# Kernel tuning notes

Measured on AMD Instinct MI355X. Metric: run time of the kernel, lower is better.

## Reference

```python
import jax, jax.numpy as jnp
import numpy as np

B, S, D, H = 2, 2048, 1024, 16
DH = D // H

def setup_inputs() -> dict:
    key = jax.random.key(0)
    ks = jax.random.split(key, 9)
    s = 1.0 / np.sqrt(D)
    def lin(k):
        kw, kb = jax.random.split(k)
        W = jax.random.uniform(kw, (D, D), jnp.float32, -s, s)
        b = jax.random.uniform(kb, (D,), jnp.float32, -s, s)
        return W, b
    Wq, bq = lin(ks[0]); Wk, bk = lin(ks[1]); Wv, bv = lin(ks[2]); Wo, bo = lin(ks[3])
    x = jax.random.normal(ks[4], (B, S, D), jnp.float32)
    return {"x": x, "Wq": Wq, "bq": bq, "Wk": Wk, "bk": bk,
            "Wv": Wv, "bv": bv, "Wo": Wo, "bo": bo}

def _split_heads(t):
    # [B,S,D] -> [B,H,S,DH]
    return t.reshape(B, S, H, DH).transpose(0, 2, 1, 3)

def reference(x, Wq, bq, Wk, bk, Wv, bv, Wo, bo):
    # torch Linear: y = x @ W.T + b
    q = _split_heads(x @ Wq.T + bq)
    k = _split_heads(x @ Wk.T + bk)
    v = _split_heads(x @ Wv.T + bv)
    scores = jnp.einsum('bhqd,bhkd->bhqk', q, k) / jnp.sqrt(jnp.float32(DH))
    p = jax.nn.softmax(scores, axis=-1)  # dropout is identity in eval
    o = jnp.einsum('bhqk,bhkd->bhqd', p, v)
    o = o.transpose(0, 2, 1, 3).reshape(B, S, D)  # combine heads
    return o @ Wo.T + bo
```

## Files before the change

### kernel.cpp

```cpp
#include <hip/hip_runtime.h>


typedef __bf16 bf16;
typedef bf16 bf16x8 __attribute__((ext_vector_type(8)));
typedef bf16 bf16x4 __attribute__((ext_vector_type(4)));
typedef short s16x4 __attribute__((ext_vector_type(4)));
typedef float f32x4 __attribute__((ext_vector_type(4)));

#define MFMA32(a, b, c) __builtin_amdgcn_mfma_f32_16x16x32_bf16(a, b, c, 0, 0, 0)

#if __has_builtin(__builtin_amdgcn_mfma_f32_16x16x16bf16_1k)
#define HAVE_MFMA16 1
#define MFMA16(a, b, c) __builtin_amdgcn_mfma_f32_16x16x16bf16_1k(a, b, c, 0, 0, 0)
#else
#define HAVE_MFMA16 0
#endif

#define GLL(g, l) __builtin_amdgcn_global_load_lds(                              \
    (const __attribute__((address_space(1))) void*)(const void*)(g),             \
    (__attribute__((address_space(3))) void*)(void*)(l), 16, 0, 0)

union pk4 { bf16x4 h; s16x4 s; unsigned int d[2]; };
union v8u { bf16x8 v; bf16x4 h[2]; s16x4 s[2]; };

__global__ __launch_bounds__(256)
void cvt_bf16(const float* __restrict__ x,  const float* __restrict__ Wq,
              const float* __restrict__ Wk, const float* __restrict__ Wv,
              const float* __restrict__ Wo,
              bf16* __restrict__ xb, bf16* __restrict__ wqb, bf16* __restrict__ wkb,
              bf16* __restrict__ wvb, bf16* __restrict__ wob)
{
    const int idx = blockIdx.x * 256 + threadIdx.x;
    const float* src; bf16* dst; int off;
    if (idx < 1048576) { src = x; dst = xb; off = idx; }
    else {
        const int r = idx - 1048576;
        const int seg = r >> 18;
        off = r & 262143;
        src = (seg == 0) ? Wq : (seg == 1) ? Wk : (seg == 2) ? Wv : Wo;
        dst = (seg == 0) ? wqb : (seg == 1) ? wkb : (seg == 2) ? wvb : wob;
    }
    const float4 v = ((const float4*)src)[off];
    bf16x4 o = {(bf16)v.x, (bf16)v.y, (bf16)v.z, (bf16)v.w};
    *(bf16x4*)(dst + (size_t)off * 4) = o;
}

__global__ __launch_bounds__(256, 3)
void qkv_gemm(const bf16* __restrict__ xb,
              const bf16* __restrict__ wqb, const float* __restrict__ bq,
              const bf16* __restrict__ wkb, const float* __restrict__ bk,
              const bf16* __restrict__ wvb, const float* __restrict__ bv,
              bf16* __restrict__ q_ws, bf16* __restrict__ k_ws, bf16* __restrict__ v_ws)
{
    const int z = blockIdx.z;
    const bf16*  W    = (z == 0) ? wqb : (z == 1) ? wkb : wvb;
    const float* bias = (z == 0) ? bq  : (z == 1) ? bk  : bv;

    __shared__ bf16 As[128][64];
    __shared__ bf16 Bs[128][64];
    __shared__ char ebuf[17408];
    bf16 (*Et)[68]  = (bf16(*)[68])ebuf;
    bf16 (*Vt)[132] = (bf16(*)[132])ebuf;

    const int m0 = blockIdx.x * 128;
    const int n0 = blockIdx.y * 128;
    const int t    = threadIdx.x;
    const int wave = t >> 6;
    const int lane = t & 63;
    const int lr   = lane & 15;
    const int quad = lane >> 4;
    const int wm = (wave & 1) * 64;
    const int wn = (wave >> 1) * 64;

    const int srow8 = lane >> 3;
    const int pcol  = (lane & 7) * 8;
    const int gcol  = ((lane & 7) ^ (lane >> 3)) * 8;
    const bf16* gaU[4]; const bf16* gbU[4]; bf16* laU[4]; bf16* lbU[4];
    #pragma unroll
    for (int u = 0; u < 4; u++) {
        const int row = wave * 32 + u * 8 + srow8;
        gaU[u] = xb + (size_t)(m0 + row) * 1024 + gcol;
        gbU[u] = W  + (size_t)(n0 + row) * 1024 + gcol;
        laU[u] = &As[row][pcol];
        lbU[u] = &Bs[row][pcol];
    }
    const int swA = (lr & 7) * 8;

    f32x4 acc[4][4] = {};

    for (int k0 = 0; k0 < 1024; k0 += 64) {
        #pragma unroll
        for (int u = 0; u < 4; u++) {
            GLL(gaU[u] + k0, laU[u]);
            GLL(gbU[u] + k0, lbU[u]);
        }
        __syncthreads();

        bf16x8 af[4][2], bfr[4][2];
        #pragma unroll
        for (int i = 0; i < 4; i++)
            #pragma unroll
            for (int kc = 0; kc < 2; kc++)
                af[i][kc] = *(const bf16x8*)&As[wm + i*16 + lr][(kc*32 + quad*8) ^ swA];
        #pragma unroll
        for (int j = 0; j < 4; j++)
            #pragma unroll
            for (int kc = 0; kc < 2; kc++)
                bfr[j][kc] = *(const bf16x8*)&Bs[wn + j*16 + lr][(kc*32 + quad*8) ^ swA];
        #pragma unroll
        for (int kc = 0; kc < 2; kc++)
            #pragma unroll
            for (int i = 0; i < 4; i++)
                #pragma unroll
                for (int j = 0; j < 4; j++)
                    acc[i][j] = MFMA32(af[i][kc], bfr[j][kc], acc[i][j]);
        __syncthreads();
    }

    const int bi = m0 >> 11, si0 = m0 & 2047;
    if (z < 2) {
        bf16* hw = (z == 0) ? q_ws : k_ws;
        const float sc = (z == 0) ? 0.125f : 1.0f;
        #pragma unroll
        for (int ph = 0; ph < 2; ph++) {
            if ((wave >> 1) == ph) {
                #pragma unroll
                for (int j = 0; j < 4; j++) {
                    const float bb = bias[n0 + ph * 64 + j * 16 + lr];
                    #pragma unroll
                    for (int i = 0; i < 4; i++)
                        #pragma unroll
                        for (int r = 0; r < 4; r++)
                            Et[wm + i*16 + quad*4 + r][j*16 + lr] =
                                (bf16)((acc[i][j][r] + bb) * sc);
                }
            }
            __syncthreads();
            const int hh = (n0 >> 6) + ph;
            bf16* dst = hw + (((size_t)bi * 16 + hh) * 2048 + si0) * 64;
            const int row = t >> 1, cc = (t & 1) * 32;
            #pragma unroll
            for (int e = 0; e < 4; e++)
                *(bf16x8*)(dst + (size_t)row * 64 + cc + e * 8) =
                    *(const bf16x8*)&Et[row][cc + e * 8];
            __syncthreads();
        }
    } else {
        #pragma unroll
        for (int ph = 0; ph < 2; ph++) {
            if ((wave >> 1) == ph) {
                #pragma unroll
                for (int j = 0; j < 4; j++) {
                    const float bb = bias[n0 + ph * 64 + j * 16 + lr];
                    #pragma unroll
                    for (int i = 0; i < 4; i++)
                        #pragma unroll
                        for (int r = 0; r < 4; r++)
                            Vt[j * 16 + lr][wm + i * 16 + quad * 4 + r] =
                                (bf16)(acc[i][j][r] + bb);
                }
            }
            __syncthreads();
            const int c  = t >> 2;
            const int sc_ = (t & 3) * 32;
            const int col = n0 + ph * 64 + c;
            const int h = col >> 6, dh = col & 63;
            bf16* dst = v_ws + (((size_t)bi * 16 + h) * 64 + dh) * 2048 + si0 + sc_;
            #pragma unroll
            for (int e = 0; e < 4; e++)
                *(bf16x8*)(dst + e * 8) = *(const bf16x8*)&Vt[c][sc_ + e * 8];
            __syncthreads();
        }
    }
}

__global__ __launch_bounds__(256, 4)
void attn(const bf16* __restrict__ q_ws, const bf16* __restrict__ k_ws,
          const bf16* __restrict__ v_ws, bf16* __restrict__ o_ws)
{
    const int qt = blockIdx.x;
    const int bh = blockIdx.y;
    const int b_ = bh >> 4, h = bh & 15;

    const bf16* qbase = q_ws + (size_t)bh * 2048 * 64;
    const bf16* kbase = k_ws + (size_t)bh * 2048 * 64;
    const bf16* vbase = v_ws + (size_t)bh * 64 * 2048;

    __shared__ bf16 Ks[128][72];
    __shared__ bf16 Vs[64][136];

    const int t    = threadIdx.x;
    const int wave = t >> 6;
    const int lane = t & 63;
    const int lr   = lane & 15;
    const int quad = lane >> 4;

    bf16x8 aq[2];
    #pragma unroll
    for (int kc = 0; kc < 2; kc++)
        aq[kc] = *(const bf16x8*)(qbase +
            (size_t)(qt*64 + wave*16 + lr) * 64 + kc*32 + quad*8);

    float m_i = -1e30f, l_i = 0.f;
    f32x4 o_accT[4] = {};
    const float C = 1.44269504f;
    const s16x4 ones = {0x3F80, 0x3F80, 0x3F80, 0x3F80};

    bf16x8 kreg[4], vreg[4];
    #pragma unroll
    for (int u = 0; u < 4; u++) {
        const int c = t + u * 256;
        kreg[u] = *(const bf16x8*)(kbase + (size_t)c * 8);
        vreg[u] = *(const bf16x8*)(vbase + (size_t)(c >> 4) * 2048 + (c & 15) * 8);
    }

    for (int kt = 0; kt < 16; kt++) {
        __syncthreads();
        #pragma unroll
        for (int u = 0; u < 4; u++) {
            const int c = t + u * 256;
            *(bf16x8*)&Ks[c >> 3][(c & 7) * 8] = kreg[u];
#if HAVE_MFMA16
            const int d = c >> 4, k_ = c & 15;
            const int lo = (k_ & 1) * 64 + (k_ >> 1) * 4;
            v8u vv; vv.v = vreg[u];
            *(bf16x4*)&Vs[d][lo]      = vv.h[0];
            *(bf16x4*)&Vs[d][lo + 32] = vv.h[1];
#else
            *(bf16x8*)&Vs[c >> 4][(c & 15) * 8] = vreg[u];
#endif
        }
        __syncthreads();
        if (kt < 15) {
            #pragma unroll
            for (int u = 0; u < 4; u++) {
                const int c = t + u * 256;
                kreg[u] = *(const bf16x8*)(kbase + (size_t)(kt+1) * 8192 + c * 8);
                vreg[u] = *(const bf16x8*)(vbase + (size_t)(c >> 4) * 2048
                                           + (kt+1) * 128 + (c & 15) * 8);
            }
        }

        f32x4 sacc[8];
        #pragma unroll
        for (int j = 0; j < 8; j++) {
            bf16x8 kf0 = *(const bf16x8*)&Ks[j*16 + lr][quad*8];
            bf16x8 kf1 = *(const bf16x8*)&Ks[j*16 + lr][32 + quad*8];
            f32x4 a = {0.f, 0.f, 0.f, 0.f};
            a = MFMA32(kf0, aq[0], a);
            a = MFMA32(kf1, aq[1], a);
            sacc[j] = a;
        }

        float m = -1e30f;
        #pragma unroll
        for (int j = 0; j < 8; j++)
            #pragma unroll
            for (int r = 0; r < 4; r++) m = fmaxf(m, sacc[j][r]);
        m = fmaxf(m, __shfl_xor(m, 16));
        m = fmaxf(m, __shfl_xor(m, 32));
        const float nm = fmaxf(m_i, m);
        const float al = exp2f((m_i - nm) * C);
        m_i = nm;
        const float nmc = nm * C;
        #pragma unroll
        for (int n = 0; n < 4; n++)
            #pragma unroll
            for (int r = 0; r < 4; r++) o_accT[n][r] *= al;

#if HAVE_MFMA16
        f32x4 lacc = {0.f, 0.f, 0.f, 0.f};
        #pragma unroll
        for (int c4 = 0; c4 < 4; c4++) {
            v8u vf[4];
            #pragma unroll
            for (int fb = 0; fb < 4; fb++)
                vf[fb].v = *(const bf16x8*)&Vs[fb*16 + lr][quad*32 + c4*8];
            #pragma unroll
            for (int jj = 0; jj < 2; jj++) {
                const int j = c4*2 + jj;
                pk4 pf;
                pf.h = bf16x4{
                    (bf16)exp2f(fmaf(sacc[j][0], C, -nmc)),
                    (bf16)exp2f(fmaf(sacc[j][1], C, -nmc)),
                    (bf16)exp2f(fmaf(sacc[j][2], C, -nmc)),
                    (bf16)exp2f(fmaf(sacc[j][3], C, -nmc))};
                #pragma unroll
                for (int fb = 0; fb < 4; fb++)
                    o_accT[fb] = MFMA16(vf[fb].s[jj], pf.s, o_accT[fb]);
                lacc = MFMA16(ones, pf.s, lacc);
            }
        }
        l_i = l_i * al + lacc[0];
#else
        float rs = 0.f;
        #pragma unroll
        for (int j = 0; j < 8; j++)
            #pragma unroll
            for (int r = 0; r < 4; r++) {
                const float p = exp2f(fmaf(sacc[j][r], C, -nmc));
                sacc[j][r] = p;
                rs += p;
            }
        rs += __shfl_xor(rs, 16);
        rs += __shfl_xor(rs, 32);
        l_i = l_i * al + rs;
        unsigned int p0[8], p1[8];
        #pragma unroll
        for (int j = 0; j < 8; j++) {
            pk4 pf;
            pf.h = bf16x4{(bf16)sacc[j][0], (bf16)sacc[j][1],
                          (bf16)sacc[j][2], (bf16)sacc[j][3]};
            p0[j] = pf.d[0]; p1[j] = pf.d[1];
        }
        const int srcA = lr + 16 * ((2 * quad) & 3);
        const int srcB = lr + 16 * ((2 * quad + 1) & 3);
        const bool hi = (quad >> 1) != 0;
        #pragma unroll
        for (int c = 0; c < 4; c++) {
            unsigned int a0 = __shfl(p0[2*c], srcA), a1 = __shfl(p0[2*c+1], srcA);
            unsigned int b0 = __shfl(p1[2*c], srcA), b1 = __shfl(p1[2*c+1], srcA);
            unsigned int c0 = __shfl(p0[2*c], srcB), c1 = __shfl(p0[2*c+1], srcB);
            unsigned int d0 = __shfl(p1[2*c], srcB), d1 = __shfl(p1[2*c+1], srcB);
            unsigned int fr[4];
            fr[0] = hi ? a1 : a0;
            fr[1] = hi ? b1 : b0;
            fr[2] = hi ? c1 : c0;
            fr[3] = hi ? d1 : d0;
            bf16x8 pf8 = *(bf16x8*)fr;
            #pragma unroll
            for (int fb = 0; fb < 4; fb++) {
                bf16x8 vf8 = *(const bf16x8*)&Vs[fb*16 + lr][c*32 + quad*8];
                o_accT[fb] = MFMA32(vf8, pf8, o_accT[fb]);
            }
        }
#endif
    }

    __syncthreads();
    bf16 (*OsE)[68] = (bf16(*)[68])&Ks[0][0];
    const float inv = 1.0f / l_i;
    const int sil = wave * 16 + lr;
    #pragma unroll
    for (int fb = 0; fb < 4; fb++)
        #pragma unroll
        for (int r = 0; r < 4; r++)
            OsE[sil][fb*16 + quad*4 + r] = (bf16)(o_accT[fb][r] * inv);
    __syncthreads();
    const int row = t >> 2, seg = (t & 3) * 16;
    bf16* dst = o_ws + ((size_t)b_ * 2048 + qt*64 + row) * 1024 + h*64 + seg;
    *(bf16x8*)(dst)     = *(const bf16x8*)&OsE[row][seg];
    *(bf16x8*)(dst + 8) = *(const bf16x8*)&OsE[row][seg + 8];
}

__global__ __launch_bounds__(256, 3)
void out_gemm(const bf16* __restrict__ o_ws,
              const bf16* __restrict__ wob, const float* __restrict__ bo,
              float* __restrict__ out)
{
    __shared__ bf16 As[64][64];
    __shared__ bf16 Bs[128][64];
    __shared__ float Ot[64][68];

    const int m0 = blockIdx.x * 64;
    const int n0 = blockIdx.y * 128;
    const int t    = threadIdx.x;
    const int wave = t >> 6;
    const int lane = t & 63;
    const int lr   = lane & 15;
    const int quad = lane >> 4;
    const int wm = (wave & 1) * 32;
    const int wn = (wave >> 1) * 64;

    const int srow8 = lane >> 3;
    const int pcol  = (lane & 7) * 8;
    const int gcol  = ((lane & 7) ^ (lane >> 3)) * 8;
    const bf16* gaU[2]; bf16* laU[2];
    #pragma unroll
    for (int u = 0; u < 2; u++) {
        const int row = wave * 16 + u * 8 + srow8;
        gaU[u] = o_ws + (size_t)(m0 + row) * 1024 + gcol;
        laU[u] = &As[row][pcol];
    }
    const bf16* gbU[4]; bf16* lbU[4];
    #pragma unroll
    for (int u = 0; u < 4; u++) {
        const int row = wave * 32 + u * 8 + srow8;
        gbU[u] = wob + (size_t)(n0 + row) * 1024 + gcol;
        lbU[u] = &Bs[row][pcol];
    }
    const int swA = (lr & 7) * 8;

    f32x4 acc[2][4] = {};

    for (int k0 = 0; k0 < 1024; k0 += 64) {
        #pragma unroll
        for (int u = 0; u < 2; u++) GLL(gaU[u] + k0, laU[u]);
        #pragma unroll
        for (int u = 0; u < 4; u++) GLL(gbU[u] + k0, lbU[u]);
        __syncthreads();

        bf16x8 af[2][2], bfr[4][2];
        #pragma unroll
        for (int i = 0; i < 2; i++)
            #pragma unroll
            for (int kc = 0; kc < 2; kc++)
                af[i][kc] = *(const bf16x8*)&As[wm + i*16 + lr][(kc*32 + quad*8) ^ swA];
        #pragma unroll
        for (int j = 0; j < 4; j++)
            #pragma unroll
            for (int kc = 0; kc < 2; kc++)
                bfr[j][kc] = *(const bf16x8*)&Bs[wn + j*16 + lr][(kc*32 + quad*8) ^ swA];
        #pragma unroll
        for (int kc = 0; kc < 2; kc++)
            #pragma unroll
            for (int i = 0; i < 2; i++)
                #pragma unroll
                for (int j = 0; j < 4; j++)
                    acc[i][j] = MFMA32(af[i][kc], bfr[j][kc], acc[i][j]);
        __syncthreads();
    }

    #pragma unroll
    for (int ph = 0; ph < 2; ph++) {
        if ((wave >> 1) == ph) {
            #pragma unroll
            for (int j = 0; j < 4; j++) {
                const float bb = bo[n0 + ph * 64 + j * 16 + lr];
                #pragma unroll
                for (int i = 0; i < 2; i++)
                    #pragma unroll
                    for (int r = 0; r < 4; r++)
                        Ot[wm + i*16 + quad*4 + r][j*16 + lr] = acc[i][j][r] + bb;
            }
        }
        __syncthreads();
        const int row = t >> 2, seg = (t & 3) * 16;
        float* dst = out + (size_t)(m0 + row) * 1024 + n0 + ph * 64 + seg;
        #pragma unroll
        for (int e = 0; e < 4; e++)
            *(float4*)(dst + e * 4) = *(const float4*)&Ot[row][seg + e * 4];
        __syncthreads();
    }
}

extern "C" void kernel_launch(void* const* d_in, const int* in_sizes, int n_in,
                              void* d_out, int out_size, void* d_ws, size_t ws_size,
                              hipStream_t stream) {
    (void)in_sizes; (void)n_in; (void)out_size; (void)ws_size;
    const float* x  = (const float*)d_in[0];
    const float* Wq = (const float*)d_in[1];
    const float* bq = (const float*)d_in[2];
    const float* Wk = (const float*)d_in[3];
    const float* bk = (const float*)d_in[4];
    const float* Wv = (const float*)d_in[5];
    const float* bv = (const float*)d_in[6];
    const float* Wo = (const float*)d_in[7];
    const float* bo = (const float*)d_in[8];
    float* out = (float*)d_out;

    char* ws = (char*)d_ws;
    const size_t MB = 1024 * 1024;
    bf16* xb   = (bf16*)(ws);
    bf16* wqb  = (bf16*)(ws + 8 * MB);
    bf16* wkb  = (bf16*)(ws + 10 * MB);
    bf16* wvb  = (bf16*)(ws + 12 * MB);
    bf16* wob  = (bf16*)(ws + 14 * MB);
    bf16* q_ws = (bf16*)(ws + 16 * MB);
    bf16* k_ws = (bf16*)(ws + 24 * MB);
    bf16* v_ws = (bf16*)(ws + 32 * MB);
    bf16* o_ws = (bf16*)(ws + 40 * MB);

    hipLaunchKernelGGL(cvt_bf16, dim3(8192), dim3(256), 0, stream,
                       x, Wq, Wk, Wv, Wo, xb, wqb, wkb, wvb, wob);
    hipLaunchKernelGGL(qkv_gemm, dim3(32, 8, 3), dim3(256), 0, stream,
                       xb, wqb, bq, wkb, bk, wvb, bv, q_ws, k_ws, v_ws);
    hipLaunchKernelGGL(attn, dim3(32, 32), dim3(256), 0, stream,
                       q_ws, k_ws, v_ws, o_ws);
    hipLaunchKernelGGL(out_gemm, dim3(64, 8), dim3(256), 0, stream,
                       o_ws, wob, bo, out);
}
```

Baseline: 230.3 us.

## Use 16x16x32 bf16 MFMA for PV and row sums in attention

Drops the 16x16x16 MFMA path in the attention kernel, which needed a transposed, split V layout in shared memory. It always uses the K=32 MFMA, building the P operand by exchanging packed bf16 probabilities across lanes with shuffles. The softmax row sum also moves to an MFMA against a ones vector, and the lane mapping for the shuffles is changed. This halves the number of PV MFMA issues and simplifies the V stores into shared memory. The cost is 32 extra cross-lane shuffles per key tile and a dependency on the shuffle mapping being correct.

```diff
diff --git a/kernel.cpp b/kernel.cpp
--- a/kernel.cpp
+++ b/kernel.cpp
@@ -4,24 +4,17 @@
 typedef __bf16 bf16;
 typedef bf16 bf16x8 __attribute__((ext_vector_type(8)));
 typedef bf16 bf16x4 __attribute__((ext_vector_type(4)));
-typedef short s16x4 __attribute__((ext_vector_type(4)));
+typedef short s16x8 __attribute__((ext_vector_type(8)));
 typedef float f32x4 __attribute__((ext_vector_type(4)));
 
 #define MFMA32(a, b, c) __builtin_amdgcn_mfma_f32_16x16x32_bf16(a, b, c, 0, 0, 0)
-
-#if __has_builtin(__builtin_amdgcn_mfma_f32_16x16x16bf16_1k)
-#define HAVE_MFMA16 1
-#define MFMA16(a, b, c) __builtin_amdgcn_mfma_f32_16x16x16bf16_1k(a, b, c, 0, 0, 0)
-#else
-#define HAVE_MFMA16 0
-#endif
 
 #define GLL(g, l) __builtin_amdgcn_global_load_lds(                              \
     (const __attribute__((address_space(1))) void*)(const void*)(g),             \
     (__attribute__((address_space(3))) void*)(void*)(l), 16, 0, 0)
 
-union pk4 { bf16x4 h; s16x4 s; unsigned int d[2]; };
-union v8u { bf16x8 v; bf16x4 h[2]; s16x4 s[2]; };
+union pk4 { bf16x4 h; unsigned int d[2]; };
+union v8s { s16x8 s; bf16x8 v; };
 
 __global__ __launch_bounds__(256)
 void cvt_bf16(const float* __restrict__ x,  const float* __restrict__ Wq,
@@ -204,7 +197,9 @@
     float m_i = -1e30f, l_i = 0.f;
     f32x4 o_accT[4] = {};
     const float C = 1.44269504f;
-    const s16x4 ones = {0x3F80, 0x3F80, 0x3F80, 0x3F80};
+    v8s ones;
+    ones.s = (s16x8){0x3F80, 0x3F80, 0x3F80, 0x3F80,
+                     0x3F80, 0x3F80, 0x3F80, 0x3F80};
 
     bf16x8 kreg[4], vreg[4];
     #pragma unroll
@@ -219,16 +214,8 @@
         #pragma unroll
         for (int u = 0; u < 4; u++) {
             const int c = t + u * 256;
-            *(bf16x8*)&Ks[c >> 3][(c & 7) * 8] = kreg[u];
-#if HAVE_MFMA16
-            const int d = c >> 4, k_ = c & 15;
-            const int lo = (k_ & 1) * 64 + (k_ >> 1) * 4;
-            v8u vv; vv.v = vreg[u];
-            *(bf16x4*)&Vs[d][lo]      = vv.h[0];
-            *(bf16x4*)&Vs[d][lo + 32] = vv.h[1];
-#else
+            *(bf16x8*)&Ks[c >> 3][(c & 7) * 8]  = kreg[u];
             *(bf16x8*)&Vs[c >> 4][(c & 15) * 8] = vreg[u];
-#endif
         }
         __syncthreads();
         if (kt < 15) {
@@ -268,54 +255,21 @@
             #pragma unroll
             for (int r = 0; r < 4; r++) o_accT[n][r] *= al;
 
-#if HAVE_MFMA16
-        f32x4 lacc = {0.f, 0.f, 0.f, 0.f};
-        #pragma unroll
-        for (int c4 = 0; c4 < 4; c4++) {
-            v8u vf[4];
-            #pragma unroll
-            for (int fb = 0; fb < 4; fb++)
-                vf[fb].v = *(const bf16x8*)&Vs[fb*16 + lr][quad*32 + c4*8];
-            #pragma unroll
-            for (int jj = 0; jj < 2; jj++) {
-                const int j = c4*2 + jj;
-                pk4 pf;
-                pf.h = bf16x4{
-                    (bf16)exp2f(fmaf(sacc[j][0], C, -nmc)),
-                    (bf16)exp2f(fmaf(sacc[j][1], C, -nmc)),
-                    (bf16)exp2f(fmaf(sacc[j][2], C, -nmc)),
-                    (bf16)exp2f(fmaf(sacc[j][3], C, -nmc))};
-                #pragma unroll
-                for (int fb = 0; fb < 4; fb++)
-                    o_accT[fb] = MFMA16(vf[fb].s[jj], pf.s, o_accT[fb]);
-                lacc = MFMA16(ones, pf.s, lacc);
-            }
-        }
-        l_i = l_i * al + lacc[0];
-#else
-        float rs = 0.f;
-        #pragma unroll
-        for (int j = 0; j < 8; j++)
-            #pragma unroll
-            for (int r = 0; r < 4; r++) {
-                const float p = exp2f(fmaf(sacc[j][r], C, -nmc));
-                sacc[j][r] = p;
-                rs += p;
-            }
-        rs += __shfl_xor(rs, 16);
-        rs += __shfl_xor(rs, 32);
-        l_i = l_i * al + rs;
         unsigned int p0[8], p1[8];
         #pragma unroll
         for (int j = 0; j < 8; j++) {
             pk4 pf;
-            pf.h = bf16x4{(bf16)sacc[j][0], (bf16)sacc[j][1],
-                          (bf16)sacc[j][2], (bf16)sacc[j][3]};
+            pf.h = bf16x4{(bf16)exp2f(fmaf(sacc[j][0], C, -nmc)),
+                          (bf16)exp2f(fmaf(sacc[j][1], C, -nmc)),
+                          (bf16)exp2f(fmaf(sacc[j][2], C, -nmc)),
+                          (bf16)exp2f(fmaf(sacc[j][3], C, -nmc))};
             p0[j] = pf.d[0]; p1[j] = pf.d[1];
         }
-        const int srcA = lr + 16 * ((2 * quad) & 3);
-        const int srcB = lr + 16 * ((2 * quad + 1) & 3);
+
+        const int srcA = lr + 32 * (quad & 1);
+        const int srcB = srcA + 16;
         const bool hi = (quad >> 1) != 0;
+        f32x4 lacc = {0.f, 0.f, 0.f, 0.f};
         #pragma unroll
         for (int c = 0; c < 4; c++) {
             unsigned int a0 = __shfl(p0[2*c], srcA), a1 = __shfl(p0[2*c+1], srcA);
@@ -333,8 +287,9 @@
                 bf16x8 vf8 = *(const bf16x8*)&Vs[fb*16 + lr][c*32 + quad*8];
                 o_accT[fb] = MFMA32(vf8, pf8, o_accT[fb]);
             }
-        }
-#endif
+            lacc = MFMA32(ones.v, pf8, lacc);
+        }
+        l_i = l_i * al + lacc[0];
     }
 
     __syncthreads();
```

Measured after the change: 237.8 us. +3.3%, slower.

## Double attention query tile per block and simplify V staging and row-sum

Applied to the files above, without the earlier changes.

The attention kernel now runs 512-thread blocks covering 128 query rows, so each K/V tile staged in shared memory serves twice as many queries. This halves global K/V traffic and the grid size. V is now stored unpermuted and read with 8-byte fragment loads for the 16x16x16 MFMA. The row-sum is computed with shuffles instead of an extra MFMA against a ones vector. The trade-offs are half as many blocks to spread across the CUs and a tighter per-thread register budget under the 512-thread launch bound.

```diff
diff --git a/kernel.cpp b/kernel.cpp
--- a/kernel.cpp
+++ b/kernel.cpp
@@ -21,7 +21,6 @@
     (__attribute__((address_space(3))) void*)(void*)(l), 16, 0, 0)
 
 union pk4 { bf16x4 h; s16x4 s; unsigned int d[2]; };
-union v8u { bf16x8 v; bf16x4 h[2]; s16x4 s[2]; };
 
 __global__ __launch_bounds__(256)
 void cvt_bf16(const float* __restrict__ x,  const float* __restrict__ Wq,
@@ -174,7 +173,7 @@
     }
 }
 
-__global__ __launch_bounds__(256, 4)
+__global__ __launch_bounds__(512, 4)
 void attn(const bf16* __restrict__ q_ws, const bf16* __restrict__ k_ws,
           const bf16* __restrict__ v_ws, bf16* __restrict__ o_ws)
 {
@@ -199,17 +198,16 @@
     #pragma unroll
     for (int kc = 0; kc < 2; kc++)
         aq[kc] = *(const bf16x8*)(qbase +
-            (size_t)(qt*64 + wave*16 + lr) * 64 + kc*32 + quad*8);
+            (size_t)(qt*128 + wave*16 + lr) * 64 + kc*32 + quad*8);
 
     float m_i = -1e30f, l_i = 0.f;
     f32x4 o_accT[4] = {};
     const float C = 1.44269504f;
-    const s16x4 ones = {0x3F80, 0x3F80, 0x3F80, 0x3F80};
-
-    bf16x8 kreg[4], vreg[4];
-    #pragma unroll
-    for (int u = 0; u < 4; u++) {
-        const int c = t + u * 256;
+
+    bf16x8 kreg[2], vreg[2];
+    #pragma unroll
+    for (int u = 0; u < 2; u++) {
+        const int c = t + u * 512;
         kreg[u] = *(const bf16x8*)(kbase + (size_t)c * 8);
         vreg[u] = *(const bf16x8*)(vbase + (size_t)(c >> 4) * 2048 + (c & 15) * 8);
     }
@@ -217,24 +215,16 @@
     for (int kt = 0; kt < 16; kt++) {
         __syncthreads();
         #pragma unroll
-        for (int u = 0; u < 4; u++) {
-            const int c = t + u * 256;
-            *(bf16x8*)&Ks[c >> 3][(c & 7) * 8] = kreg[u];
-#if HAVE_MFMA16
-            const int d = c >> 4, k_ = c & 15;
-            const int lo = (k_ & 1) * 64 + (k_ >> 1) * 4;
-            v8u vv; vv.v = vreg[u];
-            *(bf16x4*)&Vs[d][lo]      = vv.h[0];
-            *(bf16x4*)&Vs[d][lo + 32] = vv.h[1];
-#else
+        for (int u = 0; u < 2; u++) {
+            const int c = t + u * 512;
+            *(bf16x8*)&Ks[c >> 3][(c & 7) * 8]  = kreg[u];
             *(bf16x8*)&Vs[c >> 4][(c & 15) * 8] = vreg[u];
-#endif
         }
         __syncthreads();
         if (kt < 15) {
             #pragma unroll
-            for (int u = 0; u < 4; u++) {
-                const int c = t + u * 256;
+            for (int u = 0; u < 2; u++) {
+                const int c = t + u * 512;
                 kreg[u] = *(const bf16x8*)(kbase + (size_t)(kt+1) * 8192 + c * 8);
                 vreg[u] = *(const bf16x8*)(vbase + (size_t)(c >> 4) * 2048
                                            + (kt+1) * 128 + (c & 15) * 8);
@@ -263,36 +253,6 @@
         const float al = exp2f((m_i - nm) * C);
         m_i = nm;
         const float nmc = nm * C;
-        #pragma unroll
-        for (int n = 0; n < 4; n++)
-            #pragma unroll
-            for (int r = 0; r < 4; r++) o_accT[n][r] *= al;
-
-#if HAVE_MFMA16
-        f32x4 lacc = {0.f, 0.f, 0.f, 0.f};
-        #pragma unroll
-        for (int c4 = 0; c4 < 4; c4++) {
-            v8u vf[4];
-            #pragma unroll
-            for (int fb = 0; fb < 4; fb++)
-                vf[fb].v = *(const bf16x8*)&Vs[fb*16 + lr][quad*32 + c4*8];
-            #pragma unroll
-            for (int jj = 0; jj < 2; jj++) {
-                const int j = c4*2 + jj;
-                pk4 pf;
-                pf.h = bf16x4{
-                    (bf16)exp2f(fmaf(sacc[j][0], C, -nmc)),
-                    (bf16)exp2f(fmaf(sacc[j][1], C, -nmc)),
-                    (bf16)exp2f(fmaf(sacc[j][2], C, -nmc)),
-                    (bf16)exp2f(fmaf(sacc[j][3], C, -nmc))};
-                #pragma unroll
-                for (int fb = 0; fb < 4; fb++)
-                    o_accT[fb] = MFMA16(vf[fb].s[jj], pf.s, o_accT[fb]);
-                lacc = MFMA16(ones, pf.s, lacc);
-            }
-        }
-        l_i = l_i * al + lacc[0];
-#else
         float rs = 0.f;
         #pragma unroll
         for (int j = 0; j < 8; j++)
@@ -302,9 +262,29 @@
                 sacc[j][r] = p;
                 rs += p;
             }
+        #pragma unroll
+        for (int n = 0; n < 4; n++)
+            #pragma unroll
+            for (int r = 0; r < 4; r++) o_accT[n][r] *= al;
         rs += __shfl_xor(rs, 16);
         rs += __shfl_xor(rs, 32);
         l_i = l_i * al + rs;
+
+#if HAVE_MFMA16
+        #pragma unroll
+        for (int j = 0; j < 8; j++) {
+            pk4 pf;
+            pf.h = bf16x4{(bf16)sacc[j][0], (bf16)sacc[j][1],
+                          (bf16)sacc[j][2], (bf16)sacc[j][3]};
+            #pragma unroll
+            for (int fb = 0; fb < 4; fb++) {
+                pk4 vf;
+                *(unsigned long long*)vf.d =
+                    *(const unsigned long long*)&Vs[fb*16 + lr][j*16 + quad*4];
+                o_accT[fb] = MFMA16(vf.s, pf.s, o_accT[fb]);
+            }
+        }
+#else
         unsigned int p0[8], p1[8];
         #pragma unroll
         for (int j = 0; j < 8; j++) {
@@ -313,8 +293,8 @@
                           (bf16)sacc[j][2], (bf16)sacc[j][3]};
             p0[j] = pf.d[0]; p1[j] = pf.d[1];
         }
-        const int srcA = lr + 16 * ((2 * quad) & 3);
-        const int srcB = lr + 16 * ((2 * quad + 1) & 3);
+        const int srcA = lr + 32 * (quad & 1);
+        const int srcB = srcA + 16;
         const bool hi = (quad >> 1) != 0;
         #pragma unroll
         for (int c = 0; c < 4; c++) {
@@ -348,7 +328,7 @@
             OsE[sil][fb*16 + quad*4 + r] = (bf16)(o_accT[fb][r] * inv);
     __syncthreads();
     const int row = t >> 2, seg = (t & 3) * 16;
-    bf16* dst = o_ws + ((size_t)b_ * 2048 + qt*64 + row) * 1024 + h*64 + seg;
+    bf16* dst = o_ws + ((size_t)b_ * 2048 + qt*128 + row) * 1024 + h*64 + seg;
     *(bf16x8*)(dst)     = *(const bf16x8*)&OsE[row][seg];
     *(bf16x8*)(dst + 8) = *(const bf16x8*)&OsE[row][seg + 8];
 }
@@ -475,7 +455,7 @@
                        x, Wq, Wk, Wv, Wo, xb, wqb, wkb, wvb, wob);
     hipLaunchKernelGGL(qkv_gemm, dim3(32, 8, 3), dim3(256), 0, stream,
                        xb, wqb, bq, wkb, bk, wvb, bv, q_ws, k_ws, v_ws);
-    hipLaunchKernelGGL(attn, dim3(32, 32), dim3(256), 0, stream,
+    hipLaunchKernelGGL(attn, dim3(16, 32), dim3(512), 0, stream,
                        q_ws, k_ws, v_ws, o_ws);
     hipLaunchKernelGGL(out_gemm, dim3(64, 8), dim3(256), 0, stream,
                        o_ws, wob, bo, out);
```

Result: no change. 226.5 us (-1.6%).
